# Performance work log

Hardware: AMD Instinct MI355X
Metric: run time of the kernel (lower is better)

Reference implementation:

```python
import jax, jax.numpy as jnp
import numpy as np
from jax import lax

D_MODEL = 1024
D_INNER = 2048   # expand * d_model
D_STATE = 16
DT_RANK = 128    # ceil(d_inner / 16)
K = 4            # depthwise conv kernel size
EPS = 1e-5


def setup_inputs() -> dict:
    key = jax.random.key(0)
    ks = jax.random.split(key, 12)
    x = jax.random.normal(ks[0], (2, 1024, D_MODEL), dtype=jnp.float32)
    norm_w = jnp.ones((D_MODEL,), jnp.float32)
    norm_b = jnp.zeros((D_MODEL,), jnp.float32)
    # linear weights stored (in, out)
    in_proj_w = jax.random.normal(ks[1], (D_MODEL, 2 * D_INNER), jnp.float32) * (D_MODEL ** -0.5)
    conv_w = jax.random.normal(ks[2], (D_INNER, K), jnp.float32) * (K ** -0.5)
    conv_b = jnp.zeros((D_INNER,), jnp.float32)
    x_proj_w = jax.random.normal(ks[3], (D_INNER, DT_RANK + 2 * D_STATE), jnp.float32) * (D_INNER ** -0.5)
    dt_init_std = DT_RANK ** -0.5
    dt_proj_w = jax.random.uniform(ks[4], (DT_RANK, D_INNER), jnp.float32, -dt_init_std, dt_init_std)
    dt = jnp.exp(jax.random.uniform(ks[5], (D_INNER,), jnp.float32)
                 * (np.log(0.1) - np.log(0.001)) + np.log(0.001))
    dt_proj_b = dt + jnp.log(-jnp.expm1(-dt))  # inverse-softplus init
    A_log = jax.random.normal(ks[6], (D_INNER, D_STATE), jnp.float32)
    D_param = jax.random.normal(ks[7], (D_INNER,), jnp.float32)
    out_proj_w = jax.random.normal(ks[8], (D_INNER, D_MODEL), jnp.float32) * (D_INNER ** -0.5)
    return dict(x=x, norm_w=norm_w, norm_b=norm_b, in_proj_w=in_proj_w,
                conv_w=conv_w, conv_b=conv_b, x_proj_w=x_proj_w,
                dt_proj_w=dt_proj_w, dt_proj_b=dt_proj_b, A_log=A_log,
                D_param=D_param, out_proj_w=out_proj_w)


def _layer_norm(x, w, b):
    mu = jnp.mean(x, axis=-1, keepdims=True)
    var = jnp.mean(jnp.square(x - mu), axis=-1, keepdims=True)
    return (x - mu) * lax.rsqrt(var + EPS) * w + b


def _causal_depthwise_conv(x, w, b):
    # x: (B, L, D); w: (D, K). Equivalent to torch conv1d(pad=3)[:, :, :L].
    L = x.shape[1]
    xp = jnp.pad(x, ((0, 0), (K - 1, 0), (0, 0)))
    out = b
    for k in range(K):
        out = out + w[:, k] * xp[:, k:k + L, :]
    return out


def _selective_scan(u, delta, A, B, C, D):
    # u, delta: (B, L, D); A: (D, N); B, C: (B, L, N); D: (D,)
    deltaA = jnp.exp(jnp.einsum('bld,dn->bldn', delta, A))           # (B,L,D,N)
    deltaBu = jnp.einsum('bld,bln,bld->bldn', delta, B, u)           # (B,L,D,N)
    bsz, _, d, n = deltaA.shape

    def step(h, inp):
        dA, dBu, Ct = inp
        h = dA * h + dBu                                             # (B,D,N)
        y = jnp.einsum('bdn,bn->bd', h, Ct)
        return h, y

    h0 = jnp.zeros((bsz, d, n), u.dtype)
    _, ys = lax.scan(step, h0,
                     (deltaA.transpose(1, 0, 2, 3),
                      deltaBu.transpose(1, 0, 2, 3),
                      C.transpose(1, 0, 2)))
    y = ys.transpose(1, 0, 2)                                        # (B,L,D)
    return y + u * D


def reference(x, norm_w, norm_b, in_proj_w, conv_w, conv_b, x_proj_w,
              dt_proj_w, dt_proj_b, A_log, D_param, out_proj_w):
    residual = x
    h = _layer_norm(x, norm_w, norm_b)
    xr = h @ in_proj_w                                               # (B,L,2*D_inner)
    xs, res = xr[..., :D_INNER], xr[..., D_INNER:]
    xs = _causal_depthwise_conv(xs, conv_w, conv_b)
    xs = jax.nn.silu(xs)
    # S6
    A = -jnp.exp(A_log)
    xp = xs @ x_proj_w                                               # (B,L,dt_rank+2N)
    dr = xp[..., :DT_RANK]
    Bm = xp[..., DT_RANK:DT_RANK + D_STATE]
    Cm = xp[..., DT_RANK + D_STATE:]
    delta = jax.nn.softplus(dr @ dt_proj_w + dt_proj_b)
    y = _selective_scan(xs, delta, A, Bm, Cm, D_param)
    y = y * jax.nn.silu(res)
    return y @ out_proj_w + residual
```

## Files before the change

kernel.cpp:

```cpp
#include <hip/hip_runtime.h>
#include <hip/hip_bf16.h>
#include <math.h>

#define BSZ     2
#define LLEN    1024
#define DM      1024
#define DI      2048
#define DS      16
#define DTR     128
#define NXP     160
#define MROWS   (BSZ*LLEN)
#define NCH     32
#define CHL     (LLEN/NCH)

typedef short  bf16x8 __attribute__((ext_vector_type(8)));
typedef float  f32x4  __attribute__((ext_vector_type(4)));

__device__ __forceinline__ unsigned short f2bf(float f) {
    unsigned int u = __float_as_uint(f);
    return (unsigned short)((u + 0x7FFFu + ((u >> 16) & 1u)) >> 16);
}

__device__ __forceinline__ void gload_lds16(const void* g, void* lds) {
    __builtin_amdgcn_global_load_lds(
        (const __attribute__((address_space(1))) void*)g,
        (__attribute__((address_space(3))) void*)lds, 16, 0, 0);
}

__global__ __launch_bounds__(256) void ln_bf16(
    const float* __restrict__ x, const float* __restrict__ w,
    const float* __restrict__ b, unsigned short* __restrict__ hb)
{
    const int r = blockIdx.x;
    const int tid = threadIdx.x;
    const float4 v = ((const float4*)(x + (size_t)r * DM))[tid];
    float s  = v.x + v.y + v.z + v.w;
    float q  = v.x*v.x + v.y*v.y + v.z*v.z + v.w*v.w;
    #pragma unroll
    for (int o = 32; o > 0; o >>= 1) {
        s += __shfl_down(s, o);
        q += __shfl_down(q, o);
    }
    __shared__ float ss[4], sq[4];
    if ((tid & 63) == 0) { ss[tid >> 6] = s; sq[tid >> 6] = q; }
    __syncthreads();
    s = ss[0] + ss[1] + ss[2] + ss[3];
    q = sq[0] + sq[1] + sq[2] + sq[3];
    const float mu  = s * (1.0f / DM);
    const float var = q * (1.0f / DM) - mu * mu;
    const float rs  = rsqrtf(var + 1e-5f);
    const float4 wv = ((const float4*)w)[tid];
    const float4 bv = ((const float4*)b)[tid];
    ushort4 ob;
    ob.x = f2bf((v.x - mu) * rs * wv.x + bv.x);
    ob.y = f2bf((v.y - mu) * rs * wv.y + bv.y);
    ob.z = f2bf((v.z - mu) * rs * wv.z + bv.z);
    ob.w = f2bf((v.w - mu) * rs * wv.w + bv.w);
    *(ushort4*)&hb[(size_t)r * DM + (tid << 2)] = ob;
}

__global__ __launch_bounds__(256) void cast_transpose_g(
    const float* __restrict__ src, unsigned short* __restrict__ dst,
    int K, int N)
{
    __shared__ unsigned short t[64][68];
    const int tid = threadIdx.x;
    const int k0 = blockIdx.y * 64, n0 = blockIdx.x * 64;
    #pragma unroll
    for (int q = 0; q < 4; ++q) {
        int idx = q * 256 + tid;
        int r = idx >> 4, c = (idx & 15) * 4;
        if (k0 + r < K) {
            #pragma unroll
            for (int e = 0; e < 4; ++e)
                if (n0 + c + e < N)
                    t[r][c + e] = f2bf(src[(size_t)(k0 + r) * N + n0 + c + e]);
        }
    }
    __syncthreads();
    #pragma unroll
    for (int q = 0; q < 4; ++q) {
        int idx = q * 256 + tid;
        int r = idx >> 4, c = (idx & 15) * 4;
        if (n0 + r < N) {
            #pragma unroll
            for (int e = 0; e < 4; ++e)
                if (k0 + c + e < K)
                    dst[(size_t)(n0 + r) * K + k0 + c + e] = t[c + e][r];
        }
    }
}

__global__ __launch_bounds__(256) void gemm_gl(
    const unsigned short* __restrict__ A,
    const unsigned short* __restrict__ Bt,
    float* __restrict__ C, int M, int N, int K)
{
    __shared__ unsigned short As[128][64];
    __shared__ unsigned short Bs[128][64];
    const int tid  = threadIdx.x;
    const int m0   = blockIdx.y * 128;
    const int n0   = blockIdx.x * 128;
    const int wave = tid >> 6;
    const int lane = tid & 63;
    const int wr   = (wave >> 1) * 64;
    const int wc   = (wave & 1) * 64;
    const int l15  = lane & 15;
    const int kg   = lane >> 4;
    const int lrow = lane >> 3;
    const int lcol = (lane & 7) * 8;

    f32x4 acc[4][4] = {};

    for (int kt = 0; kt < K; kt += 64) {
        __syncthreads();
        #pragma unroll
        for (int q = 0; q < 4; ++q) {
            const int rbase = wave * 32 + q * 8;
            gload_lds16(&A[(size_t)(m0 + rbase + lrow) * K + kt + lcol],
                        &As[rbase][0]);
            gload_lds16(&Bt[(size_t)(n0 + rbase + lrow) * K + kt + lcol],
                        &Bs[rbase][0]);
        }
        __syncthreads();
        #pragma unroll
        for (int ks = 0; ks < 2; ++ks) {
            bf16x8 af[4], bfr[4];
            #pragma unroll
            for (int i = 0; i < 4; ++i)
                af[i] = *(const bf16x8*)&As[wr + i * 16 + l15][ks * 32 + kg * 8];
            #pragma unroll
            for (int j = 0; j < 4; ++j)
                bfr[j] = *(const bf16x8*)&Bs[wc + j * 16 + l15][ks * 32 + kg * 8];
            #pragma unroll
            for (int i = 0; i < 4; ++i)
                #pragma unroll
                for (int j = 0; j < 4; ++j)
                    acc[i][j] = __builtin_amdgcn_mfma_f32_16x16x32_bf16(
                        af[i], bfr[j], acc[i][j], 0, 0, 0);
        }
    }
    #pragma unroll
    for (int i = 0; i < 4; ++i) {
        #pragma unroll
        for (int j = 0; j < 4; ++j) {
            const int row = m0 + wr + i * 16 + kg * 4;
            const int col = n0 + wc + j * 16 + l15;
            #pragma unroll
            for (int r = 0; r < 4; ++r)
                C[(size_t)(row + r) * N + col] = acc[i][j][r];
        }
    }
}

template<int BM, int BN, int EPI>
__global__ __launch_bounds__(256) void gemm_bf16(
    const unsigned short* __restrict__ A,
    const unsigned short* __restrict__ Bt,
    float* __restrict__ C, int M, int N, int K, int kpb,
    const float* __restrict__ bias,
    const float* __restrict__ resid)
{
    constexpr int LDT = 72;
    __shared__ unsigned short As[BM][LDT];
    __shared__ unsigned short Bs[BN][LDT];
    const int tid  = threadIdx.x;
    const int m0   = blockIdx.y * BM;
    const int n0   = blockIdx.x * BN;
    const int kbeg = blockIdx.z * kpb;
    const int kend = kbeg + kpb;
    float* Cw = C + (size_t)blockIdx.z * M * N;
    const int wave = tid >> 6;
    const int lane = tid & 63;
    const int wr   = (wave >> 1) * (BM / 2);
    const int wc   = (wave & 1) * (BN / 2);
    constexpr int FM = BM / 32;
    constexpr int FN = BN / 32;
    const int l15 = lane & 15;
    const int kg  = lane >> 4;

    f32x4 acc[FM][FN] = {};

    for (int kt = kbeg; kt < kend; kt += 64) {
        __syncthreads();
        #pragma unroll
        for (int q = 0; q < BM / 32; ++q) {
            int idx = q * 256 + tid;
            int r = idx >> 3, c = (idx & 7) * 8;
            *(uint4*)&As[r][c] = *(const uint4*)&A[(size_t)(m0 + r) * K + kt + c];
        }
        #pragma unroll
        for (int q = 0; q < BN / 32; ++q) {
            int idx = q * 256 + tid;
            int r = idx >> 3, c = (idx & 7) * 8;
            *(uint4*)&Bs[r][c] = *(const uint4*)&Bt[(size_t)(n0 + r) * K + kt + c];
        }
        __syncthreads();
        #pragma unroll
        for (int ks = 0; ks < 2; ++ks) {
            bf16x8 af[FM], bfr[FN];
            #pragma unroll
            for (int i = 0; i < FM; ++i)
                af[i] = *(const bf16x8*)&As[wr + i * 16 + l15][ks * 32 + kg * 8];
            #pragma unroll
            for (int j = 0; j < FN; ++j)
                bfr[j] = *(const bf16x8*)&Bs[wc + j * 16 + l15][ks * 32 + kg * 8];
            #pragma unroll
            for (int i = 0; i < FM; ++i)
                #pragma unroll
                for (int j = 0; j < FN; ++j)
                    acc[i][j] = __builtin_amdgcn_mfma_f32_16x16x32_bf16(
                        af[i], bfr[j], acc[i][j], 0, 0, 0);
        }
    }
    #pragma unroll
    for (int i = 0; i < FM; ++i) {
        #pragma unroll
        for (int j = 0; j < FN; ++j) {
            const int row = m0 + wr + i * 16 + kg * 4;
            const int col = n0 + wc + j * 16 + l15;
            #pragma unroll
            for (int r = 0; r < 4; ++r) {
                float v = acc[i][j][r];
                if (EPI == 1) {
                    float t = v + bias[col];
                    v = (t > 20.f) ? t : log1pf(__expf(t));
                } else if (EPI == 2) {
                    v += resid[(size_t)(row + r) * N + col];
                }
                Cw[(size_t)(row + r) * N + col] = v;
            }
        }
    }
}

__global__ __launch_bounds__(256) void xproj_reduce(
    const float* __restrict__ P4, float* __restrict__ xp,
    unsigned short* __restrict__ drb)
{
    const int idx = blockIdx.x * 256 + threadIdx.x;
    float s = 0.f;
    #pragma unroll
    for (int j = 0; j < 4; ++j)
        s += P4[(size_t)j * (MROWS * NXP) + idx];
    xp[idx] = s;
    const int row = idx / NXP, col = idx - row * NXP;
    if (col < DTR) drb[(size_t)row * DTR + col] = f2bf(s);
}

__global__ __launch_bounds__(256) void conv_silu(
    const float* __restrict__ xr, const float* __restrict__ cw,
    const float* __restrict__ cb, float* __restrict__ xs,
    unsigned short* __restrict__ xsb, float* __restrict__ g)
{
    const int idx = blockIdx.x * 256 + threadIdx.x;
    const int d = idx & (DI - 1);
    const int t = (idx >> 11) & (LLEN - 1);
    const int b = idx >> 21;
    const float4 wv = ((const float4*)cw)[d];
    const float w[4] = {wv.x, wv.y, wv.z, wv.w};
    float acc = cb[d];
    #pragma unroll
    for (int k = 0; k < 4; ++k) {
        const int tt = t + k - 3;
        if (tt >= 0)
            acc = fmaf(w[k], xr[((size_t)(b * LLEN + tt) << 12) + d], acc);
    }
    const float sig = 1.f / (1.f + __expf(-acc));
    const float v = acc * sig;
    xs[idx] = v;
    xsb[idx] = f2bf(v);
    const float r = xr[((size_t)(b * LLEN + t) << 12) + DI + d];
    g[idx] = r / (1.f + __expf(-r));
}

__global__ __launch_bounds__(256) void scan_part(
    float* __restrict__ dio, float* __restrict__ xio,
    const float* __restrict__ xp, const float* __restrict__ A_log,
    const float* __restrict__ Dp, float* __restrict__ S)
{
    const int blk  = blockIdx.x;
    const int dgrp = blk & 7;
    const int j    = (blk >> 3) & (NCH - 1);
    const int b    = blk >> 8;
    const int d    = dgrp * 256 + threadIdx.x;
    float aL[DS], h[DS];
    #pragma unroll
    for (int n = 0; n < DS; ++n) {
        aL[n] = -__expf(A_log[d * DS + n]) * 1.44269504088896f;
        h[n] = 0.f;
    }
    const float Dd = Dp[d];
    float sd = 0.f;
    const int t0 = j * CHL;
    for (int t = t0; t < t0 + CHL; ++t) {
        const size_t row = (size_t)(b * LLEN + t);
        const float dlt = dio[row * DI + d];
        const float u   = xio[row * DI + d];
        const float du  = dlt * u;
        sd += dlt;
        const float* Bp = &xp[row * NXP + DTR];
        const float* Cp = Bp + DS;
        float y = Dd * u;
        #pragma unroll
        for (int n = 0; n < DS; ++n) {
            const float dA = exp2f(dlt * aL[n]);
            h[n] = fmaf(dA, h[n], du * Bp[n]);
            y = fmaf(h[n], Cp[n], y);
        }
        dio[row * DI + d] = y;
        xio[row * DI + d] = sd;
    }
    float* So = &S[(((size_t)j * BSZ + b) * DI + d) * DS];
    #pragma unroll
    for (int n = 0; n < DS; ++n) So[n] = h[n];
}

__global__ __launch_bounds__(256) void scan_fix(
    float* __restrict__ S, const float* __restrict__ cumD,
    const float* __restrict__ A_log)
{
    const int c = blockIdx.x * 256 + threadIdx.x;
    const int n = c & 15;
    const int d = (c >> 4) & (DI - 1);
    const int b = c >> 15;
    const float aL = -__expf(A_log[d * DS + n]) * 1.44269504088896f;
    float h = 0.f;
    #pragma unroll
    for (int j = 0; j < NCH; ++j) {
        const float sd = cumD[(size_t)(b * LLEN + j * CHL + CHL - 1) * DI + d];
        const size_t base = (((size_t)j * BSZ + b) * DI + d) * DS + n;
        const float Pj = exp2f(aL * sd);
        const float Sj = S[base];
        S[base] = h;
        h = fmaf(Pj, h, Sj);
    }
}

__global__ __launch_bounds__(256) void scan_corr(
    const float* __restrict__ yp, const float* __restrict__ cumD,
    const float* __restrict__ xp, const float* __restrict__ g,
    const float* __restrict__ A_log, const float* __restrict__ H0,
    unsigned short* __restrict__ yb)
{
    const int blk  = blockIdx.x;
    const int dgrp = blk & 7;
    const int j    = (blk >> 3) & (NCH - 1);
    const int b    = blk >> 8;
    const int d    = dgrp * 256 + threadIdx.x;
    float aL[DS], H[DS];
    const float* Hp = &H0[(((size_t)j * BSZ + b) * DI + d) * DS];
    #pragma unroll
    for (int n = 0; n < DS; ++n) {
        aL[n] = -__expf(A_log[d * DS + n]) * 1.44269504088896f;
        H[n] = Hp[n];
    }
    const int t0 = j * CHL;
    for (int t = t0; t < t0 + CHL; ++t) {
        const size_t row = (size_t)(b * LLEN + t);
        const float cd = cumD[row * DI + d];
        const float* Cp = &xp[row * NXP + DTR + DS];
        float corr = 0.f;
        #pragma unroll
        for (int n = 0; n < DS; ++n)
            corr = fmaf(H[n] * exp2f(aL[n] * cd), Cp[n], corr);
        const float y = yp[row * DI + d] + corr;
        yb[row * DI + d] = f2bf(y * g[row * DI + d]);
    }
}

extern "C" void kernel_launch(void* const* d_in, const int* in_sizes, int n_in,
                              void* d_out, int out_size, void* d_ws, size_t ws_size,
                              hipStream_t stream)
{
    (void)in_sizes; (void)n_in; (void)out_size; (void)ws_size;
    const float* x         = (const float*)d_in[0];
    const float* norm_w    = (const float*)d_in[1];
    const float* norm_b    = (const float*)d_in[2];
    const float* in_proj_w = (const float*)d_in[3];
    const float* conv_w    = (const float*)d_in[4];
    const float* conv_b    = (const float*)d_in[5];
    const float* x_proj_w  = (const float*)d_in[6];
    const float* dt_proj_w = (const float*)d_in[7];
    const float* dt_proj_b = (const float*)d_in[8];
    const float* A_log     = (const float*)d_in[9];
    const float* D_param   = (const float*)d_in[10];
    const float* out_proj_w= (const float*)d_in[11];
    float* out = (float*)d_out;

    char* ws = (char*)d_ws;
    float*          xr    = (float*)(ws);
    float*          P4    = (float*)(ws);
    float*          delta = (float*)(ws);
    float*          Sbuf  = (float*)(ws + 16777216);
    float*          xp    = (float*)(ws + 25165824);
    unsigned short* drb   = (unsigned short*)(ws + 27262976);
    float*          xs    = (float*)(ws + 33554432);
    float*          g     = (float*)(ws + 50331648);
    unsigned short* wInT  = (unsigned short*)(ws + 50331648);
    unsigned short* hb    = (unsigned short*)(ws + 58720256);
    unsigned short* wOutT = (unsigned short*)(ws + 58720256);
    unsigned short* xsb   = (unsigned short*)(ws + 67108864);
    unsigned short* yb    = (unsigned short*)(ws + 67108864);
    unsigned short* wXT   = (unsigned short*)(ws + 75497472);
    unsigned short* dtwT  = (unsigned short*)(ws + 76152832);

    ln_bf16<<<MROWS, 256, 0, stream>>>(x, norm_w, norm_b, hb);

    cast_transpose_g<<<dim3(64, 16), 256, 0, stream>>>(in_proj_w, wInT, DM, 2 * DI);
    cast_transpose_g<<<dim3(3, 32), 256, 0, stream>>>(x_proj_w, wXT, DI, NXP);
    cast_transpose_g<<<dim3(32, 2), 256, 0, stream>>>(dt_proj_w, dtwT, DTR, DI);

    gemm_gl<<<dim3(32, 16), 256, 0, stream>>>(hb, wInT, xr, MROWS, 2 * DI, DM);

    conv_silu<<<(BSZ * LLEN * DI) / 256, 256, 0, stream>>>(
        xr, conv_w, conv_b, xs, xsb, g);

    gemm_bf16<128, 32, 0><<<dim3(5, 16, 4), 256, 0, stream>>>(
        xsb, wXT, P4, MROWS, NXP, DI, DI / 4, nullptr, nullptr);
    xproj_reduce<<<(MROWS * NXP) / 256, 256, 0, stream>>>(P4, xp, drb);

    gemm_bf16<128, 128, 1><<<dim3(16, 16, 1), 256, 0, stream>>>(
        drb, dtwT, delta, MROWS, DI, DTR, DTR, dt_proj_b, nullptr);

    scan_part<<<BSZ * NCH * (DI / 256), 256, 0, stream>>>(
        delta, xs, xp, A_log, D_param, Sbuf);
    scan_fix<<<(BSZ * DI * DS) / 256, 256, 0, stream>>>(Sbuf, xs, A_log);
    scan_corr<<<BSZ * NCH * (DI / 256), 256, 0, stream>>>(
        delta, xs, xp, g, A_log, Sbuf, yb);

    cast_transpose_g<<<dim3(16, 32), 256, 0, stream>>>(out_proj_w, wOutT, DI, DM);

    gemm_bf16<128, 64, 2><<<dim3(16, 16, 1), 256, 0, stream>>>(
        yb, wOutT, out, MROWS, DM, DI, DI, nullptr, x);
}
```

Before: 227.9 us.

## Split scan state across thread pairs, merge weight casts, reuse templated GEMM

The chunked scan kernels now give each channel to two threads that each own 8 of the 16 state entries and combine outputs with a lane shuffle. This doubles the number of blocks and halves per-thread register state, aiming for higher occupancy and more latency hiding. The three weight cast-transposes are merged into one launch to cut launch overhead. The in_proj GEMM switches from the global-to-LDS direct-load kernel to the padded templated GEMM, which may change its speed either way.

New measurement: 215.0 us. 1.06x faster.

```diff
diff --git a/kernel.cpp b/kernel.cpp
--- a/kernel.cpp
+++ b/kernel.cpp
@@ -19,12 +19,6 @@
 __device__ __forceinline__ unsigned short f2bf(float f) {
     unsigned int u = __float_as_uint(f);
     return (unsigned short)((u + 0x7FFFu + ((u >> 16) & 1u)) >> 16);
-}
-
-__device__ __forceinline__ void gload_lds16(const void* g, void* lds) {
-    __builtin_amdgcn_global_load_lds(
-        (const __attribute__((address_space(1))) void*)g,
-        (__attribute__((address_space(3))) void*)lds, 16, 0, 0);
 }
 
 __global__ __launch_bounds__(256) void ln_bf16(
@@ -59,13 +53,22 @@
     *(ushort4*)&hb[(size_t)r * DM + (tid << 2)] = ob;
 }
 
-__global__ __launch_bounds__(256) void cast_transpose_g(
-    const float* __restrict__ src, unsigned short* __restrict__ dst,
-    int K, int N)
-{
+__global__ __launch_bounds__(256) void cast_transpose3(
+    const float* __restrict__ s0, unsigned short* __restrict__ d0_,
+    const float* __restrict__ s1, unsigned short* __restrict__ d1_,
+    const float* __restrict__ s2, unsigned short* __restrict__ d2_)
+{
+    const int bid = blockIdx.x;
+    const float* src; unsigned short* dst; int K, N, bx, by;
+    if (bid < 1024)      { src = s0; dst = d0_; K = 1024; N = 4096;
+                           bx = bid & 63; by = bid >> 6; }
+    else if (bid < 1120) { int lb = bid - 1024; src = s1; dst = d1_;
+                           K = 2048; N = 160; bx = lb % 3; by = lb / 3; }
+    else                 { int lb = bid - 1120; src = s2; dst = d2_;
+                           K = 128; N = 2048; bx = lb & 31; by = lb >> 5; }
     __shared__ unsigned short t[64][68];
     const int tid = threadIdx.x;
-    const int k0 = blockIdx.y * 64, n0 = blockIdx.x * 64;
+    const int k0 = by * 64, n0 = bx * 64;
     #pragma unroll
     for (int q = 0; q < 4; ++q) {
         int idx = q * 256 + tid;
@@ -91,64 +94,34 @@
     }
 }
 
-__global__ __launch_bounds__(256) void gemm_gl(
-    const unsigned short* __restrict__ A,
-    const unsigned short* __restrict__ Bt,
-    float* __restrict__ C, int M, int N, int K)
-{
-    __shared__ unsigned short As[128][64];
-    __shared__ unsigned short Bs[128][64];
-    const int tid  = threadIdx.x;
-    const int m0   = blockIdx.y * 128;
-    const int n0   = blockIdx.x * 128;
-    const int wave = tid >> 6;
-    const int lane = tid & 63;
-    const int wr   = (wave >> 1) * 64;
-    const int wc   = (wave & 1) * 64;
-    const int l15  = lane & 15;
-    const int kg   = lane >> 4;
-    const int lrow = lane >> 3;
-    const int lcol = (lane & 7) * 8;
-
-    f32x4 acc[4][4] = {};
-
-    for (int kt = 0; kt < K; kt += 64) {
-        __syncthreads();
-        #pragma unroll
-        for (int q = 0; q < 4; ++q) {
-            const int rbase = wave * 32 + q * 8;
-            gload_lds16(&A[(size_t)(m0 + rbase + lrow) * K + kt + lcol],
-                        &As[rbase][0]);
-            gload_lds16(&Bt[(size_t)(n0 + rbase + lrow) * K + kt + lcol],
-                        &Bs[rbase][0]);
-        }
-        __syncthreads();
-        #pragma unroll
-        for (int ks = 0; ks < 2; ++ks) {
-            bf16x8 af[4], bfr[4];
-            #pragma unroll
-            for (int i = 0; i < 4; ++i)
-                af[i] = *(const bf16x8*)&As[wr + i * 16 + l15][ks * 32 + kg * 8];
-            #pragma unroll
-            for (int j = 0; j < 4; ++j)
-                bfr[j] = *(const bf16x8*)&Bs[wc + j * 16 + l15][ks * 32 + kg * 8];
-            #pragma unroll
-            for (int i = 0; i < 4; ++i)
-                #pragma unroll
-                for (int j = 0; j < 4; ++j)
-                    acc[i][j] = __builtin_amdgcn_mfma_f32_16x16x32_bf16(
-                        af[i], bfr[j], acc[i][j], 0, 0, 0);
-        }
-    }
-    #pragma unroll
-    for (int i = 0; i < 4; ++i) {
-        #pragma unroll
-        for (int j = 0; j < 4; ++j) {
-            const int row = m0 + wr + i * 16 + kg * 4;
-            const int col = n0 + wc + j * 16 + l15;
-            #pragma unroll
-            for (int r = 0; r < 4; ++r)
-                C[(size_t)(row + r) * N + col] = acc[i][j][r];
+__global__ __launch_bounds__(256) void cast_transpose_g(
+    const float* __restrict__ src, unsigned short* __restrict__ dst,
+    int K, int N)
+{
+    __shared__ unsigned short t[64][68];
+    const int tid = threadIdx.x;
+    const int k0 = blockIdx.y * 64, n0 = blockIdx.x * 64;
+    #pragma unroll
+    for (int q = 0; q < 4; ++q) {
+        int idx = q * 256 + tid;
+        int r = idx >> 4, c = (idx & 15) * 4;
+        if (k0 + r < K) {
+            #pragma unroll
+            for (int e = 0; e < 4; ++e)
+                if (n0 + c + e < N)
+                    t[r][c + e] = f2bf(src[(size_t)(k0 + r) * N + n0 + c + e]);
+        }
+    }
+    __syncthreads();
+    #pragma unroll
+    for (int q = 0; q < 4; ++q) {
+        int idx = q * 256 + tid;
+        int r = idx >> 4, c = (idx & 15) * 4;
+        if (n0 + r < N) {
+            #pragma unroll
+            for (int e = 0; e < 4; ++e)
+                if (k0 + c + e < K)
+                    dst[(size_t)(n0 + r) * K + k0 + c + e] = t[c + e][r];
         }
     }
 }
@@ -280,14 +253,17 @@
     const float* __restrict__ Dp, float* __restrict__ S)
 {
     const int blk  = blockIdx.x;
-    const int dgrp = blk & 7;
-    const int j    = (blk >> 3) & (NCH - 1);
-    const int b    = blk >> 8;
-    const int d    = dgrp * 256 + threadIdx.x;
-    float aL[DS], h[DS];
-    #pragma unroll
-    for (int n = 0; n < DS; ++n) {
-        aL[n] = -__expf(A_log[d * DS + n]) * 1.44269504088896f;
+    const int dgrp = blk & 15;
+    const int j    = (blk >> 4) & (NCH - 1);
+    const int b    = blk >> 9;
+    const int c    = threadIdx.x >> 1;
+    const int sg   = threadIdx.x & 1;
+    const int d    = dgrp * 128 + c;
+    const int nb   = sg * 8;
+    float aL[8], h[8];
+    #pragma unroll
+    for (int n = 0; n < 8; ++n) {
+        aL[n] = -__expf(A_log[d * DS + nb + n]) * 1.44269504088896f;
         h[n] = 0.f;
     }
     const float Dd = Dp[d];
@@ -299,21 +275,24 @@
         const float u   = xio[row * DI + d];
         const float du  = dlt * u;
         sd += dlt;
-        const float* Bp = &xp[row * NXP + DTR];
-        const float* Cp = Bp + DS;
-        float y = Dd * u;
-        #pragma unroll
-        for (int n = 0; n < DS; ++n) {
+        const float* Bp = &xp[row * NXP + DTR + nb];
+        const float* Cp = &xp[row * NXP + DTR + DS + nb];
+        float y = sg ? 0.f : Dd * u;
+        #pragma unroll
+        for (int n = 0; n < 8; ++n) {
             const float dA = exp2f(dlt * aL[n]);
             h[n] = fmaf(dA, h[n], du * Bp[n]);
             y = fmaf(h[n], Cp[n], y);
         }
-        dio[row * DI + d] = y;
-        xio[row * DI + d] = sd;
-    }
-    float* So = &S[(((size_t)j * BSZ + b) * DI + d) * DS];
-    #pragma unroll
-    for (int n = 0; n < DS; ++n) So[n] = h[n];
+        y += __shfl_xor(y, 1);
+        if (!sg) {
+            dio[row * DI + d] = y;
+            xio[row * DI + d] = sd;
+        }
+    }
+    float* So = &S[(((size_t)j * BSZ + b) * DI + d) * DS + nb];
+    #pragma unroll
+    for (int n = 0; n < 8; ++n) So[n] = h[n];
 }
 
 __global__ __launch_bounds__(256) void scan_fix(
@@ -344,28 +323,34 @@
     unsigned short* __restrict__ yb)
 {
     const int blk  = blockIdx.x;
-    const int dgrp = blk & 7;
-    const int j    = (blk >> 3) & (NCH - 1);
-    const int b    = blk >> 8;
-    const int d    = dgrp * 256 + threadIdx.x;
-    float aL[DS], H[DS];
-    const float* Hp = &H0[(((size_t)j * BSZ + b) * DI + d) * DS];
-    #pragma unroll
-    for (int n = 0; n < DS; ++n) {
-        aL[n] = -__expf(A_log[d * DS + n]) * 1.44269504088896f;
+    const int dgrp = blk & 15;
+    const int j    = (blk >> 4) & (NCH - 1);
+    const int b    = blk >> 9;
+    const int c    = threadIdx.x >> 1;
+    const int sg   = threadIdx.x & 1;
+    const int d    = dgrp * 128 + c;
+    const int nb   = sg * 8;
+    float aL[8], H[8];
+    const float* Hp = &H0[(((size_t)j * BSZ + b) * DI + d) * DS + nb];
+    #pragma unroll
+    for (int n = 0; n < 8; ++n) {
+        aL[n] = -__expf(A_log[d * DS + nb + n]) * 1.44269504088896f;
         H[n] = Hp[n];
     }
     const int t0 = j * CHL;
     for (int t = t0; t < t0 + CHL; ++t) {
         const size_t row = (size_t)(b * LLEN + t);
         const float cd = cumD[row * DI + d];
-        const float* Cp = &xp[row * NXP + DTR + DS];
+        const float* Cp = &xp[row * NXP + DTR + DS + nb];
         float corr = 0.f;
         #pragma unroll
-        for (int n = 0; n < DS; ++n)
+        for (int n = 0; n < 8; ++n)
             corr = fmaf(H[n] * exp2f(aL[n] * cd), Cp[n], corr);
-        const float y = yp[row * DI + d] + corr;
-        yb[row * DI + d] = f2bf(y * g[row * DI + d]);
+        corr += __shfl_xor(corr, 1);
+        if (!sg) {
+            const float y = yp[row * DI + d] + corr;
+            yb[row * DI + d] = f2bf(y * g[row * DI + d]);
+        }
     }
 }
 
@@ -407,11 +392,11 @@
 
     ln_bf16<<<MROWS, 256, 0, stream>>>(x, norm_w, norm_b, hb);
 
-    cast_transpose_g<<<dim3(64, 16), 256, 0, stream>>>(in_proj_w, wInT, DM, 2 * DI);
-    cast_transpose_g<<<dim3(3, 32), 256, 0, stream>>>(x_proj_w, wXT, DI, NXP);
-    cast_transpose_g<<<dim3(32, 2), 256, 0, stream>>>(dt_proj_w, dtwT, DTR, DI);
-
-    gemm_gl<<<dim3(32, 16), 256, 0, stream>>>(hb, wInT, xr, MROWS, 2 * DI, DM);
+    cast_transpose3<<<1184, 256, 0, stream>>>(
+        in_proj_w, wInT, x_proj_w, wXT, dt_proj_w, dtwT);
+
+    gemm_bf16<128, 128, 0><<<dim3(32, 16, 1), 256, 0, stream>>>(
+        hb, wInT, xr, MROWS, 2 * DI, DM, DM, nullptr, nullptr);
 
     conv_silu<<<(BSZ * LLEN * DI) / 256, 256, 0, stream>>>(
         xr, conv_w, conv_b, xs, xsb, g);
@@ -423,10 +408,10 @@
     gemm_bf16<128, 128, 1><<<dim3(16, 16, 1), 256, 0, stream>>>(
         drb, dtwT, delta, MROWS, DI, DTR, DTR, dt_proj_b, nullptr);
 
-    scan_part<<<BSZ * NCH * (DI / 256), 256, 0, stream>>>(
+    scan_part<<<BSZ * NCH * (DI / 128), 256, 0, stream>>>(
         delta, xs, xp, A_log, D_param, Sbuf);
     scan_fix<<<(BSZ * DI * DS) / 256, 256, 0, stream>>>(Sbuf, xs, A_log);
-    scan_corr<<<BSZ * NCH * (DI / 256), 256, 0, stream>>>(
+    scan_corr<<<BSZ * NCH * (DI / 128), 256, 0, stream>>>(
         delta, xs, xp, g, A_log, Sbuf, yb);
 
     cast_transpose_g<<<dim3(16, 32), 256, 0, stream>>>(out_proj_w, wOutT, DI, DM);
```
